# Kernel tuning notes

Hardware: AMD Instinct MI355X
Metric: run time of the kernel (lower is better)

The kernel has to match this reference:

```python
import jax, jax.numpy as jnp
import numpy as np

B, L, D = 2, 2048, 768
HID = 32           # saliency gate hidden dim
WINDOWS = (8, 32)  # sorted window sizes
CLAMP_MIN, CLAMP_MAX = 0.05, 0.95
SCALE = 1.0 / np.sqrt(D)  # memory_dim == d_model


def setup_inputs() -> dict:
    key = jax.random.key(0)
    ks = jax.random.split(key, 16)
    s = 0.02
    return {
        "hidden_states": jax.random.normal(ks[0], (B, L, D), jnp.float32),
        "saliency_scores": jax.random.uniform(ks[1], (B, L), jnp.float32),
        # SaliencyGate MLP: Linear(1->HID), SiLU, Linear(HID->D)
        "gw1": jax.random.normal(ks[2], (HID, 1), jnp.float32) * s,
        "gb1": jnp.zeros((HID,), jnp.float32),
        "gw2": jax.random.normal(ks[3], (D, HID), jnp.float32) * s,
        "gb2": jnp.zeros((D,), jnp.float32),
        # SelectiveMemory projections
        "wq": jax.random.normal(ks[4], (D, D), jnp.float32) * s,
        "bq": jnp.zeros((D,), jnp.float32),
        "wk": jax.random.normal(ks[5], (D, D), jnp.float32) * s,
        "bk": jnp.zeros((D,), jnp.float32),
        "wv": jax.random.normal(ks[6], (D, D), jnp.float32) * s,
        "bv": jnp.zeros((D,), jnp.float32),
        "wo": jax.random.normal(ks[7], (D, D), jnp.float32) * s,
        "bo": jnp.zeros((D,), jnp.float32),
    }


def _forward(hidden_states, saliency_scores, gw1, gb1, gw2, gb2,
             wq, bq, wk, bk, wv, bv, wo, bo):
    # ---- SaliencyGate: scalar score -> MLP -> sigmoid gate -> clamp ----
    s = saliency_scores[..., None]                          # (b, l, 1)
    h1 = jax.nn.silu(s @ gw1.T + gb1)                       # (b, l, HID)
    gates = jax.nn.sigmoid(h1 @ gw2.T + gb2)                # (b, l, D)
    gates = jnp.clip(gates, CLAMP_MIN, CLAMP_MAX)
    h = hidden_states * gates

    # ---- SelectiveMemory: multi-window local attention ----
    q = h @ wq.T + bq                                       # (b, l, D)
    k = h @ wk.T + bk
    v = h @ wv.T + bv
    # Torch pads hidden_states with zeros before k/v projection; linear of a
    # zero row equals the bias, so padded key/value rows are exactly bk / bv.
    contexts = []
    for w in WINDOWS:
        kp = jnp.concatenate(
            [jnp.broadcast_to(bk, (B, w - 1, D)), k], axis=1)  # (b, l+w-1, D)
        vp = jnp.concatenate(
            [jnp.broadcast_to(bv, (B, w - 1, D)), v], axis=1)
        idx = jnp.arange(L)[:, None] + jnp.arange(w)[None, :]  # (l, w)
        kw = kp[:, idx]                                        # (b, l, w, D)
        vw = vp[:, idx]
        scores = jnp.einsum('bld,blwd->blw', q, kw) * SCALE
        attn = jax.nn.softmax(scores, axis=-1)
        contexts.append(jnp.einsum('blw,blwd->bld', attn, vw))
    merged = (contexts[0] + contexts[1]) * 0.5 if len(contexts) > 1 else contexts[0]
    return h + merged @ wo.T + bo


def reference(hidden_states, saliency_scores, gw1, gb1, gw2, gb2,
              wq, bq, wk, bk, wv, bv, wo, bo):
    return _forward(hidden_states, saliency_scores, gw1, gb1, gw2, gb2,
                    wq, bq, wk, bk, wv, bv, wo, bo)
```

## Files before the change

kernel.cpp:

```cpp
#include <hip/hip_runtime.h>
#include <hip/hip_bf16.h>
#include <stdint.h>

#define Bb 2
#define Ll 2048
#define Dd 768
#define HID 32
#define BL (Bb*Ll)
#define KPAD 32
#define KROWS (KPAD+Ll+16)

typedef __hip_bfloat16 bf16;
typedef __attribute__((ext_vector_type(8))) short short8;
typedef __attribute__((ext_vector_type(4))) short short4s;
typedef __attribute__((ext_vector_type(4))) float floatx4;

__device__ __forceinline__ float b2f(short u) {
    union { float f; unsigned i; } x; x.i = ((unsigned)(unsigned short)u) << 16; return x.f;
}
__device__ __forceinline__ bf16 f2b(float x) { return __float2bfloat16(x); }
__device__ __forceinline__ short f2bs(float x) {
    bf16 t = __float2bfloat16(x);
    union { bf16 h; short s; } u; u.h = t; return u.s;
}

typedef __attribute__((address_space(1))) const unsigned int guint;
typedef __attribute__((address_space(3))) unsigned int luint;
__device__ __forceinline__ void gload16(const bf16* g, bf16* l) {
    __builtin_amdgcn_global_load_lds((guint*)g, (luint*)l, 16, 0, 0);
}

#define CONV_VB 2304
#define KP_VB   (Bb*48)
#define VT_VB   ((Bb*Dd*48)/256)
#define PREP_VB (CONV_VB+KP_VB+VT_VB)
#define GATE_VB (BL/8)
__global__ __launch_bounds__(256) void prep_gate_kernel(
        const float* __restrict__ wq, const float* __restrict__ wk,
        const float* __restrict__ wv, const float* __restrict__ wo,
        const float* __restrict__ bk, const float* __restrict__ bv,
        const float* __restrict__ hidden, const float* __restrict__ sal,
        const float* __restrict__ gw1, const float* __restrict__ gb1,
        const float* __restrict__ gw2, const float* __restrict__ gb2,
        bf16* __restrict__ wout, bf16* __restrict__ kp, bf16* __restrict__ vT,
        bf16* __restrict__ h_b) {
    __shared__ bf16 g2t[32 * 770];
    __shared__ float h1s[8][HID];
    int bx = blockIdx.x, tid = threadIdx.x;
    if (bx < CONV_VB) {
        int idx = bx * 256 + tid;
        const int per = Dd * Dd / 4;
        int w = idx / per, r = idx % per;
        const float* src = (w == 0) ? wq : (w == 1) ? wk : (w == 2) ? wv : wo;
        float4 v = reinterpret_cast<const float4*>(src)[r];
        bf16* o = wout + (size_t)w * Dd * Dd + (size_t)r * 4;
        o[0] = f2b(v.x); o[1] = f2b(v.y); o[2] = f2b(v.z); o[3] = f2b(v.w);
    } else if (bx < CONV_VB + KP_VB) {
        int pb = bx - CONV_VB;
        int b = pb / 48, c = pb % 48;
        int row = (c < 32) ? c : (KPAD + Ll + (c - 32));
        size_t base = ((size_t)b * KROWS + row) * Dd;
        for (int i = tid; i < Dd; i += 256)
            kp[base + i] = (c < 32) ? f2b(bk[i]) : f2b(0.f);
    } else if (bx < PREP_VB) {
        int o = (bx - CONV_VB - KP_VB) * 256 + tid;
        int b = o / (Dd * 48); int rem = o - b * Dd * 48;
        int n = rem / 48, c = rem % 48;
        int col = (c < 32) ? c : (KPAD + Ll + (c - 32));
        vT[((size_t)b * Dd + n) * KROWS + col] = (c < 32) ? f2b(bv[n]) : f2b(0.f);
    } else {
        int row0 = (bx - PREP_VB) * 8;
#pragma unroll
        for (int k2 = 0; k2 < 24; ++k2) {
            int o4 = tid + k2 * 256;
            float4 v = reinterpret_cast<const float4*>(gw2)[o4];
            int d = o4 >> 3, j = (o4 & 7) * 4;
            g2t[(j + 0) * 770 + d] = f2b(v.x);
            g2t[(j + 1) * 770 + d] = f2b(v.y);
            g2t[(j + 2) * 770 + d] = f2b(v.z);
            g2t[(j + 3) * 770 + d] = f2b(v.w);
        }
        {
            int rr = tid >> 5, j = tid & 31;
            float s = sal[row0 + rr];
            float x = s * gw1[j] + gb1[j];
            h1s[rr][j] = x / (1.f + __expf(-x));
        }
        __syncthreads();
#pragma unroll
        for (int dl = 0; dl < 3; ++dl) {
            int d = tid + dl * 256;
            float base = gb2[d];
            float acc[8];
#pragma unroll
            for (int rr = 0; rr < 8; ++rr) acc[rr] = base;
#pragma unroll
            for (int j = 0; j < HID; ++j) {
                float wj = b2f(*(const short*)&g2t[j * 770 + d]);
#pragma unroll
                for (int rr = 0; rr < 8; ++rr) acc[rr] += h1s[rr][j] * wj;
            }
#pragma unroll
            for (int rr = 0; rr < 8; ++rr) {
                float g = 1.f / (1.f + __expf(-acc[rr]));
                g = fminf(fmaxf(g, 0.05f), 0.95f);
                size_t off = (size_t)(row0 + rr) * Dd + d;
                h_b[off] = f2b(hidden[off] * g);
            }
        }
    }
}

template<int NF>
__device__ __forceinline__ void gemm_core(const bf16* __restrict__ Ag, const bf16* __restrict__ Wg,
                                          int m0, int n0, bf16* As, bf16* Bs,
                                          floatx4 (&acc)[4][NF]) {
    const int tid  = threadIdx.x;
    const int wave = tid >> 6, lane = tid & 63;
    const int lrow = lane & 15, koff = (lane >> 4) * 8;
    const int wm = (wave >> 1) * 64, wn = (wave & 1) * (NF * 16);
    const char* Asb = (const char*)As;
    const char* Bsb = (const char*)Bs;

    for (int k0 = 0; k0 < Dd; k0 += 64) {
#pragma unroll
        for (int c = 0; c < 4; ++c) {
            int p = tid * 16 + c * 4096;
            int r = p >> 7;
            int o = (p & 127) ^ ((r & 7) << 4);
            gload16(Ag + (size_t)(m0 + r) * Dd + k0 + (o >> 1),
                    As + (wave * 1024 + c * 4096) / 2);
        }
#pragma unroll
        for (int c = 0; c < NF; ++c) {
            int p = tid * 16 + c * 4096;
            int r = p >> 7;
            int o = (p & 127) ^ ((r & 7) << 4);
            gload16(Wg + (size_t)(n0 + r) * Dd + k0 + (o >> 1),
                    Bs + (wave * 1024 + c * 4096) / 2);
        }
        __syncthreads();
#pragma unroll
        for (int kk = 0; kk < 64; kk += 32) {
            short8 a[4], b[NF];
#pragma unroll
            for (int i = 0; i < 4; ++i) {
                int row = wm + i * 16 + lrow;
                int byt = (row << 7) + (((kk + koff) * 2) ^ ((row & 7) << 4));
                a[i] = *reinterpret_cast<const short8*>(Asb + byt);
            }
#pragma unroll
            for (int j = 0; j < NF; ++j) {
                int row = wn + j * 16 + lrow;
                int byt = (row << 7) + (((kk + koff) * 2) ^ ((row & 7) << 4));
                b[j] = *reinterpret_cast<const short8*>(Bsb + byt);
            }
#pragma unroll
            for (int i = 0; i < 4; ++i)
#pragma unroll
                for (int j = 0; j < NF; ++j)
                    acc[i][j] = __builtin_amdgcn_mfma_f32_16x16x32_bf16(a[i], b[j], acc[i][j], 0, 0, 0);
        }
        __syncthreads();
    }
}

__global__ __launch_bounds__(256, 4) void gemm_qkv(
        const bf16* __restrict__ A, const bf16* __restrict__ W3,
        const float* __restrict__ bq, const float* __restrict__ bk, const float* __restrict__ bv,
        bf16* __restrict__ qo, bf16* __restrict__ kp, bf16* __restrict__ vT) {
    __shared__ bf16 As[128 * 64];
    __shared__ bf16 Bs[128 * 64];
    int bid = blockIdx.x;
    int xcd = bid & 7, idx = bid >> 3;
    int mtile = (xcd >> 1) * 8 + (idx & 7);
    int ntile = (xcd & 1) * 9 + (idx >> 3);
    int tgt = ntile / 6;
    int n0 = (ntile % 6) * 128;
    int m0 = mtile * 128;
    const bf16* W = W3 + (size_t)tgt * Dd * Dd;
    const float* bias = (tgt == 0) ? bq : (tgt == 1) ? bk : bv;

    floatx4 acc[4][4] = {};
    gemm_core<4>(A, W, m0, n0, As, Bs, acc);

    int wave = threadIdx.x >> 6, lane = threadIdx.x & 63;
    int wm = (wave >> 1) * 64, wn = (wave & 1) * 64;
    int crow = (lane >> 4) * 4, ccol = lane & 15;
#pragma unroll
    for (int i = 0; i < 4; ++i)
#pragma unroll
        for (int j = 0; j < 4; ++j) {
            int n = n0 + wn + j * 16 + ccol;
            float bb = bias[n];
            int m = m0 + wm + i * 16 + crow;
            int b_ = m >> 11, l = m & 2047;
            if (tgt == 2) {
                short4s pk;
#pragma unroll
                for (int rr = 0; rr < 4; ++rr) pk[rr] = f2bs(acc[i][j][rr] + bb);
                *reinterpret_cast<short4s*>(vT + ((size_t)b_ * Dd + n) * KROWS + KPAD + l) = pk;
            } else {
#pragma unroll
                for (int rr = 0; rr < 4; ++rr) {
                    size_t orow = (tgt == 0) ? (size_t)(m + rr)
                                             : ((size_t)b_ * KROWS + KPAD + l + rr);
                    bf16* outp = (tgt == 0) ? qo : kp;
                    outp[orow * Dd + n] = f2b(acc[i][j][rr] + bb);
                }
            }
        }
}

__global__ __launch_bounds__(256, 4) void gemm_out(
        const bf16* __restrict__ A, const bf16* __restrict__ W,
        const float* __restrict__ bias, const bf16* __restrict__ addend,
        float* __restrict__ out) {
    __shared__ bf16 As[128 * 64];
    __shared__ bf16 Bs[64 * 64];
    int bid = blockIdx.x;
    int xcd = bid & 7, idx = bid >> 3;
    int mtile = (xcd >> 1) * 8 + (idx & 7);
    int ntile = (xcd & 1) * 6 + (idx >> 3);
    int n0 = ntile * 64, m0 = mtile * 128;

    floatx4 acc[4][2] = {};
    gemm_core<2>(A, W, m0, n0, As, Bs, acc);

    int wave = threadIdx.x >> 6, lane = threadIdx.x & 63;
    int wm = (wave >> 1) * 64, wn = (wave & 1) * 32;
    int crow = (lane >> 4) * 4, ccol = lane & 15;
#pragma unroll
    for (int i = 0; i < 4; ++i)
#pragma unroll
        for (int j = 0; j < 2; ++j) {
            int n = n0 + wn + j * 16 + ccol;
            float bb = bias[n];
#pragma unroll
            for (int rr = 0; rr < 4; ++rr) {
                int m = m0 + wm + i * 16 + crow + rr;
                size_t o = (size_t)m * Dd + n;
                out[o] = acc[i][j][rr] + bb + b2f(*(const short*)(addend + o));
            }
        }
}

#define AW 8
__global__ __launch_bounds__(512) void attn_kernel(
        const bf16* __restrict__ q, const bf16* __restrict__ kp, const bf16* __restrict__ vT,
        bf16* __restrict__ merged) {
    __shared__ float Sp[AW][16][66];
    __shared__ bf16 wlds[AW][16 * 64];
    const int tid = threadIdx.x;
    const int wv = tid >> 6, lane = tid & 63;
    const int bid = blockIdx.x;
    const int g = (bid & 7) * 32 + (bid >> 3);
    const int b = g >> 7, L0 = (g & 127) * 16;
    const int lrow = lane & 15, koff = (lane >> 4) * 8;
    const int crow = (lane >> 4) * 4, ccol = lane & 15;
    const float scale = 0.03608439182435161f;

    const bf16* qbase = q  + ((size_t)(b * Ll + L0 + lrow)) * Dd + koff + wv * 96;
    const bf16* kbase = kp + ((size_t)b * KROWS + L0 + lrow) * Dd + koff + wv * 96;
    floatx4 s4[4] = {};
#pragma unroll
    for (int ks = 0; ks < 3; ++ks) {
        short8 a = *reinterpret_cast<const short8*>(qbase + ks * 32);
#pragma unroll
        for (int f = 0; f < 4; ++f) {
            short8 bb = *reinterpret_cast<const short8*>(kbase + (size_t)f * 16 * Dd + ks * 32);
            s4[f] = __builtin_amdgcn_mfma_f32_16x16x32_bf16(a, bb, s4[f], 0, 0, 0);
        }
    }
#pragma unroll
    for (int f = 0; f < 4; ++f)
#pragma unroll
        for (int rr = 0; rr < 4; ++rr)
            Sp[wv][crow + rr][f * 16 + ccol] = s4[f][rr];
    __syncthreads();

#pragma unroll
    for (int rr = 0; rr < 4; ++rr) {
        int r = crow + rr;
        float z[4], e[4];
#pragma unroll
        for (int f = 0; f < 4; ++f) {
            int j = f * 16 + ccol;
            float v = 0.f;
#pragma unroll
            for (int w = 0; w < AW; ++w) v += Sp[w][r][j];
            bool valid = (j >= r + 1) && (j <= r + 32);
            z[f] = valid ? v * scale : -3.0e38f;
        }
        float m = fmaxf(fmaxf(z[0], z[1]), fmaxf(z[2], z[3]));
#pragma unroll
        for (int off = 1; off < 16; off <<= 1) m = fmaxf(m, __shfl_xor(m, off));
        float S32 = 0.f, S8 = 0.f;
#pragma unroll
        for (int f = 0; f < 4; ++f) {
            e[f] = __expf(z[f] - m);
            S32 += e[f];
            int j = f * 16 + ccol;
            S8 += ((j >= r + 25) && (j <= r + 32)) ? e[f] : 0.f;
        }
#pragma unroll
        for (int off = 1; off < 16; off <<= 1) {
            S32 += __shfl_xor(S32, off);
            S8  += __shfl_xor(S8, off);
        }
        float i32 = 0.5f / S32, i8 = 0.5f / S8;
#pragma unroll
        for (int f = 0; f < 4; ++f) {
            int j = f * 16 + ccol;
            float wgt = e[f] * i32 + (((j >= r + 25) && (j <= r + 32)) ? e[f] * i8 : 0.f);
            int byt = ((r * 64 + j) * 2) ^ ((r & 7) << 4);
            *reinterpret_cast<bf16*>(reinterpret_cast<char*>(wlds[wv]) + byt) = f2b(wgt);
        }
    }

    short8 wa[2];
#pragma unroll
    for (int ks = 0; ks < 2; ++ks) {
        int byt = ((lrow * 64 + ks * 32 + koff) * 2) ^ ((lrow & 7) << 4);
        wa[ks] = *reinterpret_cast<const short8*>(reinterpret_cast<const char*>(wlds[wv]) + byt);
    }
    const bf16* vbase = vT + (size_t)b * Dd * KROWS + L0;
    bf16* obase = merged + ((size_t)(b * Ll + L0 + ccol)) * Dd;
#pragma unroll
    for (int fn = 0; fn < 6; ++fn) {
        int nr = wv * 96 + fn * 16;
        floatx4 acc = {};
#pragma unroll
        for (int ks = 0; ks < 2; ++ks) {
            short8 bb = *reinterpret_cast<const short8*>(vbase + (size_t)(nr + lrow) * KROWS + ks * 32 + koff);
            acc = __builtin_amdgcn_mfma_f32_16x16x32_bf16(bb, wa[ks], acc, 0, 0, 0);
        }
        short4s pk;
#pragma unroll
        for (int rr = 0; rr < 4; ++rr) pk[rr] = f2bs(acc[rr]);
        *reinterpret_cast<short4s*>(obase + nr + crow) = pk;
    }
}

extern "C" void kernel_launch(void* const* d_in, const int* in_sizes, int n_in,
                              void* d_out, int out_size, void* d_ws, size_t ws_size,
                              hipStream_t stream) {
    const float* hidden = (const float*)d_in[0];
    const float* sal    = (const float*)d_in[1];
    const float* gw1    = (const float*)d_in[2];
    const float* gb1    = (const float*)d_in[3];
    const float* gw2    = (const float*)d_in[4];
    const float* gb2    = (const float*)d_in[5];
    const float* wq     = (const float*)d_in[6];
    const float* bq     = (const float*)d_in[7];
    const float* wk     = (const float*)d_in[8];
    const float* bk     = (const float*)d_in[9];
    const float* wv     = (const float*)d_in[10];
    const float* bv     = (const float*)d_in[11];
    const float* wo     = (const float*)d_in[12];
    const float* bo     = (const float*)d_in[13];
    float* out = (float*)d_out;

    const size_t nBL  = (size_t)BL * Dd;
    const size_t nPad = (size_t)Bb * KROWS * Dd;
    char* p = (char*)d_ws;
    bf16* h_b = (bf16*)p; p += nBL * 2;
    bf16* q_b = (bf16*)p; p += nBL * 2;
    bf16* kpd = (bf16*)p; p += nPad * 2;
    bf16* vT  = (bf16*)p; p += nPad * 2;
    bf16* m_b = (bf16*)p; p += nBL * 2;
    bf16* w_b = (bf16*)p; p += (size_t)4 * Dd * Dd * 2;

    prep_gate_kernel<<<dim3(PREP_VB + GATE_VB), 256, 0, stream>>>(
        wq, wk, wv, wo, bk, bv, hidden, sal, gw1, gb1, gw2, gb2, w_b, kpd, vT, h_b);
    gemm_qkv<<<dim3(576), 256, 0, stream>>>(h_b, w_b, bq, bk, bv, q_b, kpd, vT);
    attn_kernel<<<dim3(256), 512, 0, stream>>>(q_b, kpd, vT, m_b);
    gemm_out<<<dim3(384), 256, 0, stream>>>(m_b, w_b + (size_t)3 * Dd * Dd, bo, h_b, out);
}
```

Measured before the change: 68.63 us.

## Retile QKV and output GEMMs to fill CUs and shrink gate LDS footprint

The QKV GEMM now uses 128x144 tiles that span the concatenated Q/K/V weight matrix, giving a 512-block grid, with each wave owning 32 rows across all 144 columns and resolving the target per 16-column fragment. The output GEMM moves to 64x96 tiles, raising its grid from 384 to 512 blocks so it covers the CUs better. The gate kernel stages gw2 in three 256-column chunks instead of all at once, cutting its shared memory so more blocks can be resident. The price is extra barriers in the gate kernel, a lower occupancy hint on the QKV GEMM, and less operand reuse per block in the output GEMM.

After: 67.87 us (median of 2 runs). No clear change (-1.1%).

```diff
diff --git a/kernel.cpp b/kernel.cpp
--- a/kernel.cpp
+++ b/kernel.cpp
@@ -44,7 +44,7 @@
         const float* __restrict__ gw2, const float* __restrict__ gb2,
         bf16* __restrict__ wout, bf16* __restrict__ kp, bf16* __restrict__ vT,
         bf16* __restrict__ h_b) {
-    __shared__ bf16 g2t[32 * 770];
+    __shared__ bf16 g2t[32 * 258];
     __shared__ float h1s[8][HID];
     int bx = blockIdx.x, tid = threadIdx.x;
     if (bx < CONV_VB) {
@@ -70,33 +70,33 @@
         vT[((size_t)b * Dd + n) * KROWS + col] = (c < 32) ? f2b(bv[n]) : f2b(0.f);
     } else {
         int row0 = (bx - PREP_VB) * 8;
-#pragma unroll
-        for (int k2 = 0; k2 < 24; ++k2) {
-            int o4 = tid + k2 * 256;
-            float4 v = reinterpret_cast<const float4*>(gw2)[o4];
-            int d = o4 >> 3, j = (o4 & 7) * 4;
-            g2t[(j + 0) * 770 + d] = f2b(v.x);
-            g2t[(j + 1) * 770 + d] = f2b(v.y);
-            g2t[(j + 2) * 770 + d] = f2b(v.z);
-            g2t[(j + 3) * 770 + d] = f2b(v.w);
-        }
         {
             int rr = tid >> 5, j = tid & 31;
             float s = sal[row0 + rr];
             float x = s * gw1[j] + gb1[j];
             h1s[rr][j] = x / (1.f + __expf(-x));
         }
-        __syncthreads();
-#pragma unroll
         for (int dl = 0; dl < 3; ++dl) {
-            int d = tid + dl * 256;
+#pragma unroll
+            for (int k2 = 0; k2 < 8; ++k2) {
+                int o4 = dl * 2048 + k2 * 256 + tid;
+                float4 v = reinterpret_cast<const float4*>(gw2)[o4];
+                int dloc = (o4 >> 3) - dl * 256;
+                int j0 = (o4 & 7) * 4;
+                g2t[(j0 + 0) * 258 + dloc] = f2b(v.x);
+                g2t[(j0 + 1) * 258 + dloc] = f2b(v.y);
+                g2t[(j0 + 2) * 258 + dloc] = f2b(v.z);
+                g2t[(j0 + 3) * 258 + dloc] = f2b(v.w);
+            }
+            __syncthreads();
+            int d = dl * 256 + tid;
             float base = gb2[d];
             float acc[8];
 #pragma unroll
             for (int rr = 0; rr < 8; ++rr) acc[rr] = base;
 #pragma unroll
             for (int j = 0; j < HID; ++j) {
-                float wj = b2f(*(const short*)&g2t[j * 770 + d]);
+                float wj = b2f(*(const short*)&g2t[j * 258 + tid]);
 #pragma unroll
                 for (int rr = 0; rr < 8; ++rr) acc[rr] += h1s[rr][j] * wj;
             }
@@ -107,20 +107,29 @@
                 size_t off = (size_t)(row0 + rr) * Dd + d;
                 h_b[off] = f2b(hidden[off] * g);
             }
-        }
-    }
-}
-
-template<int NF>
-__device__ __forceinline__ void gemm_core(const bf16* __restrict__ Ag, const bf16* __restrict__ Wg,
-                                          int m0, int n0, bf16* As, bf16* Bs,
-                                          floatx4 (&acc)[4][NF]) {
-    const int tid  = threadIdx.x;
+            __syncthreads();
+        }
+    }
+}
+
+__global__ __launch_bounds__(256, 3) void gemm_qkv(
+        const bf16* __restrict__ A, const bf16* __restrict__ W3,
+        const float* __restrict__ bq, const float* __restrict__ bk, const float* __restrict__ bv,
+        bf16* __restrict__ qo, bf16* __restrict__ kp, bf16* __restrict__ vT) {
+    __shared__ bf16 As[128 * 64];
+    __shared__ bf16 Bs[144 * 64];
+    int bid = blockIdx.x;
+    int xcd = bid & 7, idx = bid >> 3;
+    int mtile = (xcd >> 1) * 8 + (idx & 7);
+    int ntile = (xcd & 1) * 8 + (idx >> 3);
+    int m0 = mtile * 128, n0 = ntile * 144;
+    const int tid = threadIdx.x;
     const int wave = tid >> 6, lane = tid & 63;
     const int lrow = lane & 15, koff = (lane >> 4) * 8;
-    const int wm = (wave >> 1) * 64, wn = (wave & 1) * (NF * 16);
+    const int wm = wave * 32;
     const char* Asb = (const char*)As;
     const char* Bsb = (const char*)Bs;
+    floatx4 acc[2][9] = {};
 
     for (int k0 = 0; k0 < Dd; k0 += 64) {
 #pragma unroll
@@ -128,86 +137,74 @@
             int p = tid * 16 + c * 4096;
             int r = p >> 7;
             int o = (p & 127) ^ ((r & 7) << 4);
-            gload16(Ag + (size_t)(m0 + r) * Dd + k0 + (o >> 1),
+            gload16(A + (size_t)(m0 + r) * Dd + k0 + (o >> 1),
                     As + (wave * 1024 + c * 4096) / 2);
         }
 #pragma unroll
-        for (int c = 0; c < NF; ++c) {
+        for (int c = 0; c < 4; ++c) {
             int p = tid * 16 + c * 4096;
             int r = p >> 7;
             int o = (p & 127) ^ ((r & 7) << 4);
-            gload16(Wg + (size_t)(n0 + r) * Dd + k0 + (o >> 1),
+            gload16(W3 + (size_t)(n0 + r) * Dd + k0 + (o >> 1),
                     Bs + (wave * 1024 + c * 4096) / 2);
         }
+        if (tid < 128) {
+            int p = 16384 + tid * 16;
+            int r = p >> 7;
+            int o = (p & 127) ^ ((r & 7) << 4);
+            gload16(W3 + (size_t)(n0 + r) * Dd + k0 + (o >> 1),
+                    Bs + (16384 + wave * 1024) / 2);
+        }
         __syncthreads();
 #pragma unroll
         for (int kk = 0; kk < 64; kk += 32) {
-            short8 a[4], b[NF];
-#pragma unroll
-            for (int i = 0; i < 4; ++i) {
+            short8 a[2], b[9];
+#pragma unroll
+            for (int i = 0; i < 2; ++i) {
                 int row = wm + i * 16 + lrow;
                 int byt = (row << 7) + (((kk + koff) * 2) ^ ((row & 7) << 4));
                 a[i] = *reinterpret_cast<const short8*>(Asb + byt);
             }
 #pragma unroll
-            for (int j = 0; j < NF; ++j) {
-                int row = wn + j * 16 + lrow;
+            for (int j = 0; j < 9; ++j) {
+                int row = j * 16 + lrow;
                 int byt = (row << 7) + (((kk + koff) * 2) ^ ((row & 7) << 4));
                 b[j] = *reinterpret_cast<const short8*>(Bsb + byt);
             }
 #pragma unroll
-            for (int i = 0; i < 4; ++i)
-#pragma unroll
-                for (int j = 0; j < NF; ++j)
+            for (int i = 0; i < 2; ++i)
+#pragma unroll
+                for (int j = 0; j < 9; ++j)
                     acc[i][j] = __builtin_amdgcn_mfma_f32_16x16x32_bf16(a[i], b[j], acc[i][j], 0, 0, 0);
         }
         __syncthreads();
     }
-}
-
-__global__ __launch_bounds__(256, 4) void gemm_qkv(
-        const bf16* __restrict__ A, const bf16* __restrict__ W3,
-        const float* __restrict__ bq, const float* __restrict__ bk, const float* __restrict__ bv,
-        bf16* __restrict__ qo, bf16* __restrict__ kp, bf16* __restrict__ vT) {
-    __shared__ bf16 As[128 * 64];
-    __shared__ bf16 Bs[128 * 64];
-    int bid = blockIdx.x;
-    int xcd = bid & 7, idx = bid >> 3;
-    int mtile = (xcd >> 1) * 8 + (idx & 7);
-    int ntile = (xcd & 1) * 9 + (idx >> 3);
-    int tgt = ntile / 6;
-    int n0 = (ntile % 6) * 128;
-    int m0 = mtile * 128;
-    const bf16* W = W3 + (size_t)tgt * Dd * Dd;
-    const float* bias = (tgt == 0) ? bq : (tgt == 1) ? bk : bv;
-
-    floatx4 acc[4][4] = {};
-    gemm_core<4>(A, W, m0, n0, As, Bs, acc);
-
-    int wave = threadIdx.x >> 6, lane = threadIdx.x & 63;
-    int wm = (wave >> 1) * 64, wn = (wave & 1) * 64;
+
     int crow = (lane >> 4) * 4, ccol = lane & 15;
 #pragma unroll
-    for (int i = 0; i < 4; ++i)
-#pragma unroll
-        for (int j = 0; j < 4; ++j) {
-            int n = n0 + wn + j * 16 + ccol;
-            float bb = bias[n];
+    for (int i = 0; i < 2; ++i)
+#pragma unroll
+        for (int j = 0; j < 9; ++j) {
+            int nf = n0 + j * 16;
+            int tgt = nf / 768;
+            int nn = nf - tgt * 768 + ccol;
+            const float* bias = (tgt == 0) ? bq : (tgt == 1) ? bk : bv;
+            float bb = bias[nn];
             int m = m0 + wm + i * 16 + crow;
             int b_ = m >> 11, l = m & 2047;
             if (tgt == 2) {
                 short4s pk;
 #pragma unroll
                 for (int rr = 0; rr < 4; ++rr) pk[rr] = f2bs(acc[i][j][rr] + bb);
-                *reinterpret_cast<short4s*>(vT + ((size_t)b_ * Dd + n) * KROWS + KPAD + l) = pk;
+                *reinterpret_cast<short4s*>(vT + ((size_t)b_ * Dd + nn) * KROWS + KPAD + l) = pk;
+            } else if (tgt == 1) {
+#pragma unroll
+                for (int rr = 0; rr < 4; ++rr)
+                    kp[((size_t)b_ * KROWS + KPAD + l + rr) * Dd + nn] = f2b(acc[i][j][rr] + bb);
             } else {
 #pragma unroll
-                for (int rr = 0; rr < 4; ++rr) {
-                    size_t orow = (tgt == 0) ? (size_t)(m + rr)
-                                             : ((size_t)b_ * KROWS + KPAD + l + rr);
-                    bf16* outp = (tgt == 0) ? qo : kp;
-                    outp[orow * Dd + n] = f2b(acc[i][j][rr] + bb);
-                }
+                for (int rr = 0; rr < 4; ++rr)
+                    qo[(size_t)(m + rr) * Dd + nn] = f2b(acc[i][j][rr] + bb);
             }
         }
 }
@@ -216,24 +213,68 @@
         const bf16* __restrict__ A, const bf16* __restrict__ W,
         const float* __restrict__ bias, const bf16* __restrict__ addend,
         float* __restrict__ out) {
-    __shared__ bf16 As[128 * 64];
-    __shared__ bf16 Bs[64 * 64];
+    __shared__ bf16 As[64 * 64];
+    __shared__ bf16 Bs[96 * 64];
     int bid = blockIdx.x;
     int xcd = bid & 7, idx = bid >> 3;
-    int mtile = (xcd >> 1) * 8 + (idx & 7);
-    int ntile = (xcd & 1) * 6 + (idx >> 3);
-    int n0 = ntile * 64, m0 = mtile * 128;
-
-    floatx4 acc[4][2] = {};
-    gemm_core<2>(A, W, m0, n0, As, Bs, acc);
-
-    int wave = threadIdx.x >> 6, lane = threadIdx.x & 63;
-    int wm = (wave >> 1) * 64, wn = (wave & 1) * 32;
+    int mtile = (xcd >> 1) * 16 + (idx & 15);
+    int ntile = (xcd & 1) * 4 + (idx >> 4);
+    int m0 = mtile * 64, n0 = ntile * 96;
+    const int tid = threadIdx.x;
+    const int wave = tid >> 6, lane = tid & 63;
+    const int lrow = lane & 15, koff = (lane >> 4) * 8;
+    const int wm = (wave >> 1) * 32, wn = (wave & 1) * 48;
+    const char* Asb = (const char*)As;
+    const char* Bsb = (const char*)Bs;
+    floatx4 acc[2][3] = {};
+
+    for (int k0 = 0; k0 < Dd; k0 += 64) {
+#pragma unroll
+        for (int c = 0; c < 2; ++c) {
+            int p = tid * 16 + c * 4096;
+            int r = p >> 7;
+            int o = (p & 127) ^ ((r & 7) << 4);
+            gload16(A + (size_t)(m0 + r) * Dd + k0 + (o >> 1),
+                    As + (wave * 1024 + c * 4096) / 2);
+        }
+#pragma unroll
+        for (int c = 0; c < 3; ++c) {
+            int p = tid * 16 + c * 4096;
+            int r = p >> 7;
+            int o = (p & 127) ^ ((r & 7) << 4);
+            gload16(W + (size_t)(n0 + r) * Dd + k0 + (o >> 1),
+                    Bs + (wave * 1024 + c * 4096) / 2);
+        }
+        __syncthreads();
+#pragma unroll
+        for (int kk = 0; kk < 64; kk += 32) {
+            short8 a[2], b[3];
+#pragma unroll
+            for (int i = 0; i < 2; ++i) {
+                int row = wm + i * 16 + lrow;
+                int byt = (row << 7) + (((kk + koff) * 2) ^ ((row & 7) << 4));
+                a[i] = *reinterpret_cast<const short8*>(Asb + byt);
+            }
+#pragma unroll
+            for (int j = 0; j < 3; ++j) {
+                int row = wn + j * 16 + lrow;
+                int byt = (row << 7) + (((kk + koff) * 2) ^ ((row & 7) << 4));
+                b[j] = *reinterpret_cast<const short8*>(Bsb + byt);
+            }
+#pragma unroll
+            for (int i = 0; i < 2; ++i)
+#pragma unroll
+                for (int j = 0; j < 3; ++j)
+                    acc[i][j] = __builtin_amdgcn_mfma_f32_16x16x32_bf16(a[i], b[j], acc[i][j], 0, 0, 0);
+        }
+        __syncthreads();
+    }
+
     int crow = (lane >> 4) * 4, ccol = lane & 15;
 #pragma unroll
-    for (int i = 0; i < 4; ++i)
-#pragma unroll
-        for (int j = 0; j < 2; ++j) {
+    for (int i = 0; i < 2; ++i)
+#pragma unroll
+        for (int j = 0; j < 3; ++j) {
             int n = n0 + wn + j * 16 + ccol;
             float bb = bias[n];
 #pragma unroll
@@ -373,7 +414,7 @@
 
     prep_gate_kernel<<<dim3(PREP_VB + GATE_VB), 256, 0, stream>>>(
         wq, wk, wv, wo, bk, bv, hidden, sal, gw1, gb1, gw2, gb2, w_b, kpd, vT, h_b);
-    gemm_qkv<<<dim3(576), 256, 0, stream>>>(h_b, w_b, bq, bk, bv, q_b, kpd, vT);
+    gemm_qkv<<<dim3(512), 256, 0, stream>>>(h_b, w_b, bq, bk, bv, q_b, kpd, vT);
     attn_kernel<<<dim3(256), 512, 0, stream>>>(q_b, kpd, vT, m_b);
-    gemm_out<<<dim3(384), 256, 0, stream>>>(m_b, w_b + (size_t)3 * Dd * Dd, bo, h_b, out);
-}
+    gemm_out<<<dim3(512), 256, 0, stream>>>(m_b, w_b + (size_t)3 * Dd * Dd, bo, h_b, out);
+}
```
